# Optimization experiments

Hardware: AMD Instinct MI355X
Metric: run time of the kernel (lower is better)

Reference implementation:

```python
import jax, jax.numpy as jnp
import numpy as np

N = 200_000   # total nodes across batched AIGs
E = 400_000   # edges (fan-in ~2 per gate)
D = 64        # input_dim == dim_hidden (required by in-place scatter in _gru_forward)
B = 16        # number of graphs in batch
LF = 12       # num forward topological levels
LB = 12       # num backward topological levels
NUM_ROUNDS = 1


def setup_inputs() -> dict:
    key = jax.random.key(0)
    ks = jax.random.split(key, 9)
    node_type = jax.random.randint(ks[0], (N,), 0, 3, dtype=jnp.int32)
    num_inverted_predecessors = jax.random.randint(ks[1], (N,), 0, 3, dtype=jnp.int32)
    edge_index = jax.random.randint(ks[2], (2, E), 0, N, dtype=jnp.int32)
    forward_level = jax.random.randint(ks[3], (N,), 0, LF, dtype=jnp.int32)
    backward_level = jax.random.randint(ks[4], (N,), 0, LB, dtype=jnp.int32)
    batch = jnp.sort(jax.random.randint(ks[5], (N,), 0, B, dtype=jnp.int32))
    s = 1.0 / np.sqrt(D)
    W_enc = jax.random.normal(ks[6], (2, D), dtype=jnp.float32) * 0.5
    b_enc = jnp.zeros((D,), dtype=jnp.float32)
    W_f = jax.random.normal(ks[7], (D, D), dtype=jnp.float32) * s
    b_f = jnp.zeros((D,), dtype=jnp.float32)
    W_b = jax.random.normal(ks[8], (D, D), dtype=jnp.float32) * s
    b_b = jnp.zeros((D,), dtype=jnp.float32)
    return dict(node_type=node_type,
                num_inverted_predecessors=num_inverted_predecessors,
                edge_index=edge_index,
                forward_level=forward_level,
                backward_level=backward_level,
                batch=batch,
                W_enc=W_enc, b_enc=b_enc,
                W_f=W_f, b_f=b_f,
                W_b=W_b, b_b=b_b)


def reference(node_type, num_inverted_predecessors, edge_index,
              forward_level, backward_level, batch,
              W_enc, b_enc, W_f, b_f, W_b, b_b):
    # h_init = node_encoder(cat(node_type, num_inverted_predecessors))
    x = jnp.stack([node_type, num_inverted_predecessors], axis=1).astype(W_enc.dtype)  # [N,2]
    h = x @ W_enc + b_enc  # [N,D] node_state
    src, dst = edge_index[0], edge_index[1]

    for _ in range(NUM_ROUNDS):
        # forward topological sweep: level l nodes receive sum of mlp(h_src)
        # over incoming edges whose destination is at level l (subgraph dim=1).
        for l in range(1, LF):
            m = h @ W_f + b_f                                    # AggConv mlp on current state
            e_w = (forward_level[dst] == l).astype(h.dtype)      # edges into level-l nodes
            msg = jax.ops.segment_sum(m[src] * e_w[:, None], dst, num_segments=N)
            h = jnp.where((forward_level == l)[:, None], msg, h)  # scatter l_msg into node_state
        # backward sweep (reverse flow): level-l sources receive sum of
        # mlp_b(h_dst) over outgoing edges (subgraph dim=0, target_to_source).
        for l in range(1, LB):
            m = h @ W_b + b_b
            e_w = (backward_level[src] == l).astype(h.dtype)
            msg = jax.ops.segment_sum(m[dst] * e_w[:, None], src, num_segments=N)
            h = jnp.where((backward_level == l)[:, None], msg, h)

    # readout over output nodes (node_type == 1): [global_max_pool, global_add_pool]
    out_mask = (node_type == 1)
    neg_inf = jnp.finfo(h.dtype).min
    max_pool = jax.ops.segment_max(jnp.where(out_mask[:, None], h, neg_inf), batch, num_segments=B)
    sum_pool = jax.ops.segment_sum(h * out_mask[:, None].astype(h.dtype), batch, num_segments=B)
    return jnp.concatenate([max_pool, sum_pool], axis=1)  # [B, 2*D]
```

## Files before the change

### kernel.cpp

```cpp
#include <hip/hip_runtime.h>
#include <float.h>

#define NLVL 12
#define NB   16
#define NBLK 256


struct Params {
    const int *nt, *ninv, *src, *dst, *fl, *bl, *batch;
    const float *We, *be, *Wf, *bf, *Wb, *bb;
    float *hN, *hB, *tabg, *out;
    int *rowptr, *cursor, *col, *nb_f, *nb_b, *onodes, *bsums, *meta, *plarr;
    int *cntf, *cntb, *cnto, *blkf, *blkb, *blko;
    int N, E, M, outN;
};

__device__ __forceinline__ float rlanef(float x, int l) {
    return __int_as_float(__builtin_amdgcn_readlane(__float_as_int(x), l));
}

__global__ void k_deg_hist(Params p) {
    __shared__ int hf[NLVL], hb[NLVL], ho[NB];
    int tid = threadIdx.x, bid = blockIdx.x;
    if (tid < NLVL) { hf[tid] = 0; hb[tid] = 0; }
    if (tid < NB) ho[tid] = 0;
    __syncthreads();
    int g = bid * 256 + tid, gs = gridDim.x * 256;
    for (int e = g; e < p.E; e += gs) {
        atomicAdd(&p.rowptr[p.dst[e]], 1);
        atomicAdd(&p.rowptr[p.N + p.src[e]], 1);
    }
    int chunk = (p.N + gridDim.x - 1) / gridDim.x;
    int lo = bid * chunk, hi = lo + chunk; if (hi > p.N) hi = p.N;
    for (int i = lo + tid; i < hi; i += 256) {
        int f = p.fl[i], b = p.bl[i];
        int t = p.nt[i], iv = p.ninv[i];
        p.plarr[i] = f | (b << 4) | ((t * 3 + iv) << 8);
        atomicAdd(&hf[f], 1);
        atomicAdd(&hb[b], 1);
        if (t == 1) atomicAdd(&ho[p.batch[i]], 1);
    }
    __syncthreads();
    if (tid < NLVL) { p.cntf[tid * NBLK + bid] = hf[tid]; p.cntb[tid * NBLK + bid] = hb[tid]; }
    if (tid < NB) p.cnto[tid * NBLK + bid] = ho[tid];
}

__global__ void k_scan1(int* __restrict__ data, int M, int* __restrict__ bsums) {
    __shared__ int s[512];
    int t = threadIdx.x;
    int g = blockIdx.x * 512 + t;
    int v = (g < M) ? data[g] : 0;
    s[t] = v;
    __syncthreads();
    for (int off = 1; off < 512; off <<= 1) {
        int add = (t >= off) ? s[t - off] : 0;
        __syncthreads();
        s[t] += add;
        __syncthreads();
    }
    if (g < M) data[g] = s[t] - v;
    if (t == 511) bsums[blockIdx.x] = s[511];
}

__global__ void k_scan_top(int* __restrict__ bsums, int nblk, Params p,
                           float* __restrict__ out, int outN) {
    __shared__ int s[1024];
    __shared__ int tot[48];
    int t = threadIdx.x;
    int* meta = p.meta;
    for (int i = t; i < outN; i += 1024)
        out[i] = ((i & 127) < 64) ? -FLT_MAX : 0.0f;
    if (t < 576) {
        int row = t >> 6, j = t & 63;
        float nf = (float)(row / 3), iv = (float)(row % 3);
        p.tabg[t] = fmaf(nf, p.We[j], fmaf(iv, p.We[64 + j], p.be[j]));
    }
    int seg = t >> 8, b = t & 255;
    for (int r = 0; r < 3; r++) {
        int l = 4 * r + seg;
        int v = p.cntf[l * NBLK + b];
        s[t] = v; __syncthreads();
        for (int off = 1; off < NBLK; off <<= 1) {
            int add = (b >= off) ? s[t - off] : 0; __syncthreads();
            s[t] += add; __syncthreads();
        }
        p.blkf[l * NBLK + b] = s[t] - v;
        if (b == NBLK - 1) tot[l] = s[t];
        __syncthreads();
    }
    for (int r = 0; r < 3; r++) {
        int l = 4 * r + seg;
        int v = p.cntb[l * NBLK + b];
        s[t] = v; __syncthreads();
        for (int off = 1; off < NBLK; off <<= 1) {
            int add = (b >= off) ? s[t - off] : 0; __syncthreads();
            s[t] += add; __syncthreads();
        }
        p.blkb[l * NBLK + b] = s[t] - v;
        if (b == NBLK - 1) tot[16 + l] = s[t];
        __syncthreads();
    }
    for (int r = 0; r < 4; r++) {
        int l = 4 * r + seg;
        int v = p.cnto[l * NBLK + b];
        s[t] = v; __syncthreads();
        for (int off = 1; off < NBLK; off <<= 1) {
            int add = (b >= off) ? s[t - off] : 0; __syncthreads();
            s[t] += add; __syncthreads();
        }
        p.blko[l * NBLK + b] = s[t] - v;
        if (b == NBLK - 1) tot[32 + l] = s[t];
        __syncthreads();
    }
    if (t == 0) { int a = 0; for (int l = 0; l < NLVL; l++) { meta[96 + l] = a; a += tot[l]; } meta[96 + NLVL] = a; }
    if (t == 1) { int a = 0; for (int l = 0; l < NLVL; l++) { meta[128 + l] = a; a += tot[16 + l]; } meta[128 + NLVL] = a; }
    if (t == 2) { int a = 0; for (int l = 0; l < NB; l++) { meta[160 + l] = a; a += tot[32 + l]; } meta[160 + NB] = a; }
    __syncthreads();
    for (int i = t; i < NLVL * NBLK; i += 1024) p.blkf[i] += meta[96 + (i >> 8)];
    for (int i = t; i < NLVL * NBLK; i += 1024) p.blkb[i] += meta[128 + (i >> 8)];
    for (int i = t; i < NB * NBLK; i += 1024) p.blko[i] += meta[160 + (i >> 8)];
    int v = (t < nblk) ? bsums[t] : 0;
    s[t] = v;
    __syncthreads();
    for (int off = 1; off < 1024; off <<= 1) {
        int add = (t >= off) ? s[t - off] : 0;
        __syncthreads();
        s[t] += add;
        __syncthreads();
    }
    if (t < nblk) bsums[t] = s[t] - v;
}

__global__ void k_scan_add(int* __restrict__ rowptr, int* __restrict__ cursor, int M, int total,
                           const int* __restrict__ bsums) {
    int g = blockIdx.x * blockDim.x + threadIdx.x;
    if (g >= M) return;
    int r = rowptr[g] + bsums[g >> 9];
    rowptr[g] = r;
    cursor[g] = r;
    if (g == 0) rowptr[M] = total;
}

__global__ void k_fill(Params p) {
    __shared__ int cur[48];
    int tid = threadIdx.x, bid = blockIdx.x;
    int g = bid * 256 + tid, gs = gridDim.x * 256;
    int N = p.N;

    for (int e = g; e < p.E; e += gs) {
        int s = p.src[e], d = p.dst[e];
        p.col[atomicAdd(&p.cursor[d], 1)] = s | (p.plarr[s] << 18);
        p.col[atomicAdd(&p.cursor[N + s], 1)] = d | (p.plarr[d] << 18);
    }

    if (tid < NLVL) { cur[tid] = p.blkf[tid * NBLK + bid]; cur[16 + tid] = p.blkb[tid * NBLK + bid]; }
    if (tid < NB) cur[32 + tid] = p.blko[tid * NBLK + bid];
    __syncthreads();
    int chunk = (N + gridDim.x - 1) / gridDim.x;
    int lo = bid * chunk, hi = lo + chunk; if (hi > N) hi = N;
    for (int i = lo + tid; i < hi; i += 256) {
        int pl = p.plarr[i];
        int lf = pl & 15, lb = (pl >> 4) & 15, tx = (pl >> 8) & 15;
        int pk = i | (pl << 18);
        p.nb_f[atomicAdd(&cur[lf], 1)] = pk;
        p.nb_b[atomicAdd(&cur[16 + lb], 1)] = pk;
        if (tx >= 3 && tx < 6)
            p.onodes[atomicAdd(&cur[32 + p.batch[i]], 1)] = pk;
    }
}

__global__ __launch_bounds__(256, 4) void k_sweep(Params p, int lvl, int dir) {
    const int tid = threadIdx.x, lane = tid & 63;
    const float* W = dir ? p.Wb : p.Wf;
    float w[64];
    #pragma unroll
    for (int k = 0; k < 64; k++) w[k] = W[k * 64 + lane];
    float bv = (dir ? p.bb : p.bf)[lane];

    const int* nb = dir ? p.nb_b : p.nb_f;
    const int* rp = p.rowptr + (dir ? p.N : 0);
    int start = p.meta[(dir ? 128 : 96) + lvl];
    int cnt   = p.meta[(dir ? 128 : 96) + lvl + 1] - start;
    const int wid = (blockIdx.x * 256 + tid) >> 6;
    const int nw  = (gridDim.x * 256) >> 6;
    const int q = lane >> 4, fb = (lane & 15) * 4;
    float* db = dir ? p.hB : p.hN;

    int c0 = (int)((long long)cnt * wid / nw);
    int c1 = (int)((long long)cnt * (wid + 1) / nw);
    for (int i = c0; i < c1; i += 4) {
        int my = i + q;
        int v = 0, rpv = 0, rpe = 0;
        if (my < c1) {
            int e = nb[start + my];
            v = e & 0x3FFFF;
            rpv = rp[v]; rpe = rp[v + 1];
        }
        float4 acc = make_float4(0.f, 0.f, 0.f, 0.f);
        for (int cb = rpv; cb < rpe; cb++) {
            int cu = p.col[cb];
            int u = cu & 0x3FFFF;
            int flu = (cu >> 18) & 15, blu = (cu >> 22) & 15;
            const float* sp;
            if (dir == 0)
                sp = (flu > 0 && flu < lvl) ? (p.hN + (size_t)u * 64)
                                            : (p.tabg + ((cu >> 26) & 15) * 64);
            else
                sp = (blu > 0 && blu < lvl) ? (p.hB + (size_t)u * 64)
                   : (flu > 0)              ? (p.hN + (size_t)u * 64)
                                            : (p.tabg + ((cu >> 26) & 15) * 64);
            const float4 x = *(const float4*)(sp + fb);
            acc.x += x.x; acc.y += x.y; acc.z += x.z; acc.w += x.w;
        }
        #pragma unroll
        for (int qq = 0; qq < 4; qq++) {
            if (i + qq >= c1) break;
            int vs   = __builtin_amdgcn_readlane(v, 16 * qq);
            int degs = __builtin_amdgcn_readlane(rpe, 16 * qq)
                     - __builtin_amdgcn_readlane(rpv, 16 * qq);
            float o = bv * (float)degs;
            #pragma unroll
            for (int m = 0; m < 16; m++) {
                float ax = rlanef(acc.x, 16 * qq + m);
                float ay = rlanef(acc.y, 16 * qq + m);
                float az = rlanef(acc.z, 16 * qq + m);
                float aw = rlanef(acc.w, 16 * qq + m);
                o = fmaf(ax, w[4 * m + 0], o);
                o = fmaf(ay, w[4 * m + 1], o);
                o = fmaf(az, w[4 * m + 2], o);
                o = fmaf(aw, w[4 * m + 3], o);
            }
            db[(size_t)vs * 64 + lane] = o;
        }
    }
}

__device__ inline void atomicMaxF(float* addr, float val) {
    int* ai = (int*)addr;
    int old = *ai;
    while (__int_as_float(old) < val) {
        int assumed = old;
        old = atomicCAS(ai, assumed, __float_as_int(val));
        if (old == assumed) break;
    }
}

__global__ void k_readout(Params p) {
    int lane = threadIdx.x & 63;
    int b = blockIdx.x >> 5;
    int sl = blockIdx.x & 31;
    int a0 = p.meta[160 + b], a1 = p.meta[161 + b];
    int cnt = a1 - a0;
    if (cnt == 0) return;
    int lo = a0 + (int)((long long)cnt * sl / 32);
    int hi = a0 + (int)((long long)cnt * (sl + 1) / 32);
    int wcnt = hi - lo;
    int wave = threadIdx.x >> 6;
    int wl = lo + (wcnt * wave) / 4;
    int wh = lo + (wcnt * (wave + 1)) / 4;
    if (wh <= wl) return;
    float mx = -FLT_MAX, sm = 0.f;
    for (int k = wl; k < wh; k += 64) {
        int take = wh - k; if (take > 64) take = 64;
        int el = (lane < take) ? p.onodes[k + lane] : 0;
        for (int j = 0; j < take; j++) {
            int e = __shfl(el, j, 64);
            int v = e & 0x3FFFF;
            int flv = (e >> 18) & 15, blv = (e >> 22) & 15;
            const float* sp = (blv > 0) ? (p.hB + (size_t)v * 64)
                            : (flv > 0) ? (p.hN + (size_t)v * 64)
                                        : (p.tabg + ((e >> 26) & 15) * 64);
            float x = sp[lane];
            mx = fmaxf(mx, x);
            sm += x;
        }
    }
    atomicMaxF(&p.out[b * 128 + lane], mx);
    atomicAdd(&p.out[b * 128 + 64 + lane], sm);
}

extern "C" void kernel_launch(void* const* d_in, const int* in_sizes, int n_in,
                              void* d_out, int out_size, void* d_ws, size_t ws_size,
                              hipStream_t stream) {
    int N = in_sizes[0];
    int E = in_sizes[2] / 2;
    int M = 2 * N;

    Params p;
    p.nt    = (const int*)d_in[0];
    p.ninv  = (const int*)d_in[1];
    p.src   = (const int*)d_in[2];
    p.dst   = (const int*)d_in[2] + E;
    p.fl    = (const int*)d_in[3];
    p.bl    = (const int*)d_in[4];
    p.batch = (const int*)d_in[5];
    p.We    = (const float*)d_in[6];
    p.be    = (const float*)d_in[7];
    p.Wf    = (const float*)d_in[8];
    p.bf    = (const float*)d_in[9];
    p.Wb    = (const float*)d_in[10];
    p.bb    = (const float*)d_in[11];
    p.out   = (float*)d_out;
    p.N = N; p.E = E; p.M = M; p.outN = out_size;

    char* ws = (char*)d_ws;
    size_t off = 0;
    auto alloc = [&](size_t bytes) -> char* {
        char* q = ws + off;
        off = (off + bytes + 255) & ~(size_t)255;
        return q;
    };
    p.rowptr = (int*)  alloc((size_t)(M + 1) * sizeof(int));
    p.meta   = (int*)  alloc(256 * sizeof(int));
    size_t zbytes = (size_t)((char*)(p.meta + 256) - (char*)p.rowptr);
    p.hN     = (float*)alloc((size_t)N * 64 * sizeof(float));
    p.hB     = (float*)alloc((size_t)N * 64 * sizeof(float));
    p.tabg   = (float*)alloc(9 * 64 * sizeof(float));
    p.cursor = (int*)  alloc((size_t)M * sizeof(int));
    p.col    = (int*)  alloc((size_t)2 * E * sizeof(int));
    p.nb_f   = (int*)  alloc((size_t)N * sizeof(int));
    p.nb_b   = (int*)  alloc((size_t)N * sizeof(int));
    p.onodes = (int*)  alloc((size_t)N * sizeof(int));
    p.plarr  = (int*)  alloc((size_t)N * sizeof(int));
    p.bsums  = (int*)  alloc(1024 * sizeof(int));
    p.cntf   = (int*)  alloc(NLVL * NBLK * sizeof(int));
    p.cntb   = (int*)  alloc(NLVL * NBLK * sizeof(int));
    p.cnto   = (int*)  alloc(NB * NBLK * sizeof(int));
    p.blkf   = (int*)  alloc(NLVL * NBLK * sizeof(int));
    p.blkb   = (int*)  alloc(NLVL * NBLK * sizeof(int));
    p.blko   = (int*)  alloc(NB * NBLK * sizeof(int));

    int nscan = (M + 511) / 512;

    hipMemsetAsync(p.rowptr, 0, zbytes, stream);
    k_deg_hist<<<NBLK, 256, 0, stream>>>(p);
    k_scan1<<<nscan, 512, 0, stream>>>(p.rowptr, M, p.bsums);
    k_scan_top<<<1, 1024, 0, stream>>>(p.bsums, nscan, p, p.out, out_size);
    k_scan_add<<<(M + 255) / 256, 256, 0, stream>>>(p.rowptr, p.cursor, M, 2 * E, p.bsums);
    k_fill<<<NBLK, 256, 0, stream>>>(p);

    for (int l = 1; l < NLVL; l++)
        k_sweep<<<1024, 256, 0, stream>>>(p, l, 0);
    for (int l = 1; l < NLVL; l++)
        k_sweep<<<1024, 256, 0, stream>>>(p, l, 1);

    k_readout<<<NB * 32, 256, 0, stream>>>(p);
}
```

Measured before the change: 478.0 us.

## Partition edge atomics by node range across 512 blocks for cache locality

```diff
diff --git a/kernel.cpp b/kernel.cpp
--- a/kernel.cpp
+++ b/kernel.cpp
@@ -4,6 +4,7 @@
 #define NLVL 12
 #define NB   16
 #define NBLK 256
+#define GEDGE 512
 
 
 struct Params {
@@ -25,24 +26,31 @@
     if (tid < NLVL) { hf[tid] = 0; hb[tid] = 0; }
     if (tid < NB) ho[tid] = 0;
     __syncthreads();
-    int g = bid * 256 + tid, gs = gridDim.x * 256;
-    for (int e = g; e < p.E; e += gs) {
-        atomicAdd(&p.rowptr[p.dst[e]], 1);
-        atomicAdd(&p.rowptr[p.N + p.src[e]], 1);
-    }
-    int chunk = (p.N + gridDim.x - 1) / gridDim.x;
-    int lo = bid * chunk, hi = lo + chunk; if (hi > p.N) hi = p.N;
-    for (int i = lo + tid; i < hi; i += 256) {
-        int f = p.fl[i], b = p.bl[i];
-        int t = p.nt[i], iv = p.ninv[i];
-        p.plarr[i] = f | (b << 4) | ((t * 3 + iv) << 8);
-        atomicAdd(&hf[f], 1);
-        atomicAdd(&hb[b], 1);
-        if (t == 1) atomicAdd(&ho[p.batch[i]], 1);
-    }
-    __syncthreads();
-    if (tid < NLVL) { p.cntf[tid * NBLK + bid] = hf[tid]; p.cntb[tid * NBLK + bid] = hb[tid]; }
-    if (tid < NB) p.cnto[tid * NBLK + bid] = ho[tid];
+    int part = bid & 7;
+    int plo = (int)(((long long)p.N * part) >> 3);
+    int phi = (int)(((long long)p.N * (part + 1)) >> 3);
+    int sb = bid >> 3;
+    for (int e = sb * 256 + tid; e < p.E; e += (GEDGE / 8) * 256) {
+        int d = p.dst[e];
+        if (d >= plo && d < phi) atomicAdd(&p.rowptr[d], 1);
+        int s = p.src[e];
+        if (s >= plo && s < phi) atomicAdd(&p.rowptr[p.N + s], 1);
+    }
+    if (bid < NBLK) {
+        int chunk = (p.N + NBLK - 1) / NBLK;
+        int lo = bid * chunk, hi = lo + chunk; if (hi > p.N) hi = p.N;
+        for (int i = lo + tid; i < hi; i += 256) {
+            int f = p.fl[i], b = p.bl[i];
+            int t = p.nt[i], iv = p.ninv[i];
+            p.plarr[i] = f | (b << 4) | ((t * 3 + iv) << 8);
+            atomicAdd(&hf[f], 1);
+            atomicAdd(&hb[b], 1);
+            if (t == 1) atomicAdd(&ho[p.batch[i]], 1);
+        }
+        __syncthreads();
+        if (tid < NLVL) { p.cntf[tid * NBLK + bid] = hf[tid]; p.cntb[tid * NBLK + bid] = hb[tid]; }
+        if (tid < NB) p.cnto[tid * NBLK + bid] = ho[tid];
+    }
 }
 
 __global__ void k_scan1(int* __restrict__ data, int M, int* __restrict__ bsums) {
@@ -144,19 +152,25 @@
 __global__ void k_fill(Params p) {
     __shared__ int cur[48];
     int tid = threadIdx.x, bid = blockIdx.x;
-    int g = bid * 256 + tid, gs = gridDim.x * 256;
     int N = p.N;
 
-    for (int e = g; e < p.E; e += gs) {
+    int part = bid & 7;
+    int plo = (int)(((long long)N * part) >> 3);
+    int phi = (int)(((long long)N * (part + 1)) >> 3);
+    int sb = bid >> 3;
+    for (int e = sb * 256 + tid; e < p.E; e += (GEDGE / 8) * 256) {
         int s = p.src[e], d = p.dst[e];
-        p.col[atomicAdd(&p.cursor[d], 1)] = s | (p.plarr[s] << 18);
-        p.col[atomicAdd(&p.cursor[N + s], 1)] = d | (p.plarr[d] << 18);
-    }
-
+        if (d >= plo && d < phi)
+            p.col[atomicAdd(&p.cursor[d], 1)] = s | (p.plarr[s] << 18);
+        if (s >= plo && s < phi)
+            p.col[atomicAdd(&p.cursor[N + s], 1)] = d | (p.plarr[d] << 18);
+    }
+
+    if (bid >= NBLK) return;
     if (tid < NLVL) { cur[tid] = p.blkf[tid * NBLK + bid]; cur[16 + tid] = p.blkb[tid * NBLK + bid]; }
     if (tid < NB) cur[32 + tid] = p.blko[tid * NBLK + bid];
     __syncthreads();
-    int chunk = (N + gridDim.x - 1) / gridDim.x;
+    int chunk = (N + NBLK - 1) / NBLK;
     int lo = bid * chunk, hi = lo + chunk; if (hi > N) hi = N;
     for (int i = lo + tid; i < hi; i += 256) {
         int pl = p.plarr[i];
@@ -333,11 +347,11 @@
     int nscan = (M + 511) / 512;
 
     hipMemsetAsync(p.rowptr, 0, zbytes, stream);
-    k_deg_hist<<<NBLK, 256, 0, stream>>>(p);
+    k_deg_hist<<<GEDGE, 256, 0, stream>>>(p);
     k_scan1<<<nscan, 512, 0, stream>>>(p.rowptr, M, p.bsums);
     k_scan_top<<<1, 1024, 0, stream>>>(p.bsums, nscan, p, p.out, out_size);
     k_scan_add<<<(M + 255) / 256, 256, 0, stream>>>(p.rowptr, p.cursor, M, 2 * E, p.bsums);
-    k_fill<<<NBLK, 256, 0, stream>>>(p);
+    k_fill<<<GEDGE, 256, 0, stream>>>(p);
 
     for (int l = 1; l < NLVL; l++)
         k_sweep<<<1024, 256, 0, stream>>>(p, l, 0);
```

New measurement: 483.1 us. No clear change (+1.1%).
